# Kernel tuning notes

Measured on AMD Instinct MI355X. Metric: run time of the kernel, lower is better.

The kernel has to match this reference:

```python
import jax, jax.numpy as jnp
import numpy as np


def setup_inputs() -> dict:
    key = jax.random.key(0)
    ks = jax.random.split(key, 9)
    B, C, H, W = 4, 256, 64, 64
    Ci = C // 2
    s = 0.05  # keep activations numerically tame
    return {
        "x": jax.random.normal(ks[0], (B, C, H, W), jnp.float32),
        "w_g": jax.random.normal(ks[1], (Ci, C), jnp.float32) * s,
        "b_g": jax.random.normal(ks[2], (Ci,), jnp.float32) * s,
        "w_theta": jax.random.normal(ks[3], (Ci, C), jnp.float32) * s,
        "b_theta": jax.random.normal(ks[4], (Ci,), jnp.float32) * s,
        "w_phi": jax.random.normal(ks[5], (Ci, C), jnp.float32) * s,
        "b_phi": jax.random.normal(ks[6], (Ci,), jnp.float32) * s,
        "w_out": jax.random.normal(ks[7], (C, Ci), jnp.float32) * s,
        "b_out": jax.random.normal(ks[8], (C,), jnp.float32) * s,
    }


def reference(x, w_g, b_g, w_theta, b_theta, w_phi, b_phi, w_out, b_out):
    B, C, H, W = x.shape
    Ci = w_g.shape[0]
    N = H * W
    xr = x.reshape(B, C, N)  # flatten spatial dims

    def proj(w, b):  # 1x1 conv == per-pixel GEMM
        return jnp.einsum("oc,bcn->bon", w, xr) + b[None, :, None]

    g_x = proj(w_g, b_g)          # [B, Ci, N]
    theta_x = proj(w_theta, b_theta)
    phi_x = proj(w_phi, b_phi)

    scale = jnp.asarray(Ci, x.dtype) ** 0.5
    f = jnp.einsum("bci,bcj->bij", theta_x, phi_x) / scale  # [B, N, N]
    attn = jax.nn.softmax(f, axis=-1)

    # out[b,c,i] = sum_j g_x[b,c,j] * attn[b,i,j]
    out = jnp.einsum("bcj,bij->bci", g_x, attn)             # [B, Ci, N]
    y = jnp.einsum("oc,bcn->bon", w_out, out) + b_out[None, :, None]
    return y.reshape(B, C, H, W) + x
```

## Files before the change

### kernel.cpp

```cpp
#include <hip/hip_runtime.h>
#include <hip/hip_bf16.h>


typedef float f32x4 __attribute__((ext_vector_type(4)));
typedef short s16x8 __attribute__((ext_vector_type(8)));

#define B_  4
#define C_  256
#define CI_ 128
#define N_  4096

#define OFF_XT   0ull
#define OFF_Q    (8ull  << 20)
#define OFF_K    (12ull << 20)
#define OFF_G    (16ull << 20)
#define OFF_O    (20ull << 20)
#define OFF_WQK  (24ull << 20)
#define OFF_WG   (OFF_WQK + 131072)
#define OFF_WOUT (OFF_WG  + 65536)
#define OFF_BQK  (OFF_WOUT + 65536)
#define OFF_BG   (OFF_BQK + 1024)
#define OFF_BOUT (OFF_BG  + 512)
#define OFF_END  (OFF_BOUT + 1024)

__device__ inline f32x4 mfma16(s16x8 a, s16x8 b, f32x4 c) {
    return __builtin_amdgcn_mfma_f32_16x16x32_bf16(a, b, c, 0, 0, 0);
}
__device__ inline s16x8 ld8(const __hip_bfloat16* p) { return *(const s16x8*)p; }
__device__ inline float b2f(short u) {
    return __uint_as_float(((unsigned int)(unsigned short)u) << 16);
}
__device__ inline unsigned int pk2(float a, float b) {
    __hip_bfloat162 h;
    h.x = __float2bfloat16(a); h.y = __float2bfloat16(b);
    return *(unsigned int*)&h;
}
__device__ inline void gload_lds16(const void* g, void* l) {
    __builtin_amdgcn_global_load_lds(
        (const __attribute__((address_space(1))) unsigned int*)g,
        (__attribute__((address_space(3))) unsigned int*)l, 16, 0, 0);
}
__device__ inline float fexp2(float x) { return __builtin_amdgcn_exp2f(x); }

__global__ void prep_weights(const float* wg, const float* bg,
                             const float* wt, const float* bt,
                             const float* wp, const float* bp,
                             const float* wo, const float* bo, char* ws) {
    __hip_bfloat16* Wqk  = (__hip_bfloat16*)(ws + OFF_WQK);
    __hip_bfloat16* Wg   = (__hip_bfloat16*)(ws + OFF_WG);
    __hip_bfloat16* Wout = (__hip_bfloat16*)(ws + OFF_WOUT);
    float* Bqk  = (float*)(ws + OFF_BQK);
    float* Bg   = (float*)(ws + OFF_BG);
    float* Bout = (float*)(ws + OFF_BOUT);
    const float rs = 0.08838834764831845f * 1.4426950408889634f;
    int idx = blockIdx.x * 256 + threadIdx.x;
    if (idx < 65536) {
        int r = idx >> 8, c = idx & 255;
        float v = (r < 128) ? wt[r * 256 + c] * rs : wp[(r - 128) * 256 + c];
        Wqk[idx] = __float2bfloat16(v);
    }
    if (idx < 32768) {
        Wg[idx]   = __float2bfloat16(wg[idx]);
        Wout[idx] = __float2bfloat16(wo[idx]);
    }
    if (idx < 256) { Bqk[idx] = (idx < 128) ? bt[idx] * rs : bp[idx - 128]; Bout[idx] = bo[idx]; }
    if (idx < 128) Bg[idx] = bg[idx];
}

__global__ __launch_bounds__(256) void transpose_x(const float* x, char* ws) {
    __shared__ float tile[32][33];
    __hip_bfloat16* XT = (__hip_bfloat16*)(ws + OFF_XT);
    int b = blockIdx.z;
    int n0 = blockIdx.x * 32, c0 = blockIdx.y * 32;
    int tx = threadIdx.x & 31, ty = threadIdx.x >> 5;
#pragma unroll
    for (int r = 0; r < 4; r++)
        tile[ty + 8 * r][tx] = x[(size_t)(b * C_ + c0 + ty + 8 * r) * N_ + n0 + tx];
    __syncthreads();
#pragma unroll
    for (int r = 0; r < 4; r++)
        XT[(size_t)(b * N_ + n0 + ty + 8 * r) * C_ + c0 + tx] =
            __float2bfloat16(tile[tx][ty + 8 * r]);
}

__global__ __launch_bounds__(256) void proj(char* ws) {
    const __hip_bfloat16* XT  = (const __hip_bfloat16*)(ws + OFF_XT);
    const __hip_bfloat16* Wqk = (const __hip_bfloat16*)(ws + OFF_WQK);
    const __hip_bfloat16* Wg  = (const __hip_bfloat16*)(ws + OFF_WG);
    const float* Bqk = (const float*)(ws + OFF_BQK);
    const float* Bg  = (const float*)(ws + OFF_BG);
    __hip_bfloat16* Q  = (__hip_bfloat16*)(ws + OFF_Q);
    __hip_bfloat16* Kb = (__hip_bfloat16*)(ws + OFF_K);
    __hip_bfloat16* G  = (__hip_bfloat16*)(ws + OFF_G);

    __shared__ char at[32 * 512];

    int b = blockIdx.y, n0 = blockIdx.x * 32;
    int w = threadIdx.x >> 6, l = threadIdx.x & 63, lr = l & 15, lg = l >> 4;

    const char* xbase = (const char*)(XT + ((size_t)b * N_ + n0) * C_);
#pragma unroll
    for (int p = 0; p < 4; p++) {
        int row = p * 8 + w * 2 + (l >> 5);
        int slot = l & 31;
        const char* src = xbase + row * 512 + ((slot ^ (row & 7)) << 4);
        gload_lds16(src, &at[(p * 8 + w * 2) * 512]);
    }
    __syncthreads();

    f32x4 acc[4][2] = {};
    f32x4 accg[2][2] = {};
    int o0q = w * 64, o0g = w * 32;
#pragma unroll
    for (int kk = 0; kk < 8; kk++) {
        s16x8 a[2];
#pragma unroll
        for (int nf = 0; nf < 2; nf++) {
            int row = nf * 16 + lr;
            int s = (4 * kk + lg) ^ (row & 7);
            a[nf] = *(const s16x8*)(&at[row * 512 + s * 16]);
        }
#pragma unroll
        for (int of = 0; of < 4; of++) {
            s16x8 bb = ld8(Wqk + (size_t)(o0q + 16 * of + lr) * C_ + kk * 32 + lg * 8);
            acc[of][0] = mfma16(a[0], bb, acc[of][0]);
            acc[of][1] = mfma16(a[1], bb, acc[of][1]);
        }
#pragma unroll
        for (int og = 0; og < 2; og++) {
            s16x8 ag = ld8(Wg + (size_t)(o0g + 16 * og + lr) * C_ + kk * 32 + lg * 8);
            accg[og][0] = mfma16(ag, a[0], accg[og][0]);
            accg[og][1] = mfma16(ag, a[1], accg[og][1]);
        }
    }
#pragma unroll
    for (int of = 0; of < 4; of++) {
        int o = o0q + 16 * of + lr;
        float bias = Bqk[o];
#pragma unroll
        for (int nf = 0; nf < 2; nf++) {
#pragma unroll
            for (int i = 0; i < 4; i++) {
                int n = n0 + 16 * nf + lg * 4 + i;
                float v = acc[of][nf][i] + bias;
                if (o < 128) Q [(size_t)(b * N_ + n) * CI_ + o]         = __float2bfloat16(v);
                else         Kb[(size_t)(b * N_ + n) * CI_ + (o - 128)] = __float2bfloat16(v);
            }
        }
    }
#pragma unroll
    for (int og = 0; og < 2; og++) {
#pragma unroll
        for (int i = 0; i < 4; i++) {
            int o = o0g + 16 * og + lg * 4 + i;
            float bias = Bg[o];
#pragma unroll
            for (int nf = 0; nf < 2; nf++) {
                int n = n0 + 16 * nf + lr;
                G[(size_t)(b * CI_ + o) * N_ + n] = __float2bfloat16(accg[og][nf][i] + bias);
            }
        }
    }
}

__global__ __launch_bounds__(256, 3) void flash6(char* ws, int nchunk,
                                                 unsigned long long off_part,
                                                 unsigned long long off_ml) {
    const __hip_bfloat16* Q  = (const __hip_bfloat16*)(ws + OFF_Q);
    const __hip_bfloat16* Kb = (const __hip_bfloat16*)(ws + OFF_K);
    const __hip_bfloat16* G  = (const __hip_bfloat16*)(ws + OFF_G);
    __hip_bfloat16* OP = (__hip_bfloat16*)(ws + off_part);
    float* ML = (float*)(ws + off_ml);

    __shared__ char kbuf[2][32 * 256];
    __shared__ char vbuf[2][128 * 64];
    __shared__ char pbuf[4][2][2048];

    int L = blockIdx.x;
    int npairs = B_ * nchunk;
    int pair = L % npairs, qt = L / npairs;
    int b = pair / nchunk, cz = pair % nchunk;
    int per = 128 / nchunk, rem = 128 % nchunk;
    int jb_t = per * cz + (cz < rem ? cz : rem);
    int sz_t = per + (cz < rem ? 1 : 0);
    int jb = jb_t << 5, je = jb + (sz_t << 5);

    int w = threadIdx.x >> 6, l = threadIdx.x & 63, lr = l & 15, lg = l >> 4;
    int q0 = qt * 128 + w * 32;
    int swz = (lr & 7) << 4;
    char* pw = &pbuf[w][0][0];

    auto STAGE = [&](int pb_, int j0_) {
#pragma unroll
        for (int i = 0; i < 2; i++) {
            int row = w * 8 + i * 4 + (l >> 4);
            int bcol = ((l & 15) << 4) ^ ((row & 7) << 4);
            const char* src = (const char*)Kb + (((size_t)b * N_ + j0_ + row) << 8) + bcol;
            gload_lds16(src, &kbuf[pb_][(w * 8 + i * 4) * 256]);
        }
#pragma unroll
        for (int i = 0; i < 2; i++) {
            int c = w * 32 + i * 16 + (l >> 2);
            int joct = l & 3;
            const char* src = (const char*)G + ((((size_t)b * CI_ + c) * N_ + j0_) << 1)
                              + ((joct ^ (c & 3)) << 4);
            gload_lds16(src, &vbuf[pb_][(w * 32 + i * 16) * 64]);
        }
    };

    s16x8 qa[2][4];
#pragma unroll
    for (int qf = 0; qf < 2; qf++) {
        const __hip_bfloat16* qrow = Q + ((size_t)b * N_ + q0 + 16 * qf + lr) * CI_ + lg * 8;
#pragma unroll
        for (int kk = 0; kk < 4; kk++) qa[qf][kk] = ld8(qrow + kk * 32);
    }

    f32x4 oacc[2][8] = {};
    float m_i[2], lsum[2] = {0.f, 0.f};

    STAGE(0, jb);
    __syncthreads();
    int pb = 0;

    for (int j0 = jb; j0 < je; j0 += 32) {
        if (j0 + 32 < je) STAGE(pb ^ 1, j0 + 32);
        const char* kb = kbuf[pb];
        const char* vbb = vbuf[pb];
        f32x4 s[2][2] = {};
        __builtin_amdgcn_s_setprio(1);
#pragma unroll
        for (int kk = 0; kk < 4; kk++) {
            int bc = ((kk << 6) + (lg << 4)) ^ swz;
            s16x8 kf0 = *(const s16x8*)(kb + lr * 256 + bc);
            s16x8 kf1 = *(const s16x8*)(kb + (16 + lr) * 256 + bc);
            s[0][0] = mfma16(kf0, qa[0][kk], s[0][0]);
            s[1][0] = mfma16(kf0, qa[1][kk], s[1][0]);
            s[0][1] = mfma16(kf1, qa[0][kk], s[0][1]);
            s[1][1] = mfma16(kf1, qa[1][kk], s[1][1]);
        }
        __builtin_amdgcn_s_setprio(0);
        if (j0 == jb) {
#pragma unroll
            for (int qf = 0; qf < 2; qf++) {
                f32x4 m4;
                m4[0] = fmaxf(s[qf][0][0], s[qf][1][0]);
                m4[1] = fmaxf(s[qf][0][1], s[qf][1][1]);
                m4[2] = fmaxf(s[qf][0][2], s[qf][1][2]);
                m4[3] = fmaxf(s[qf][0][3], s[qf][1][3]);
                float tm = fmaxf(fmaxf(m4[0], m4[1]), fmaxf(m4[2], m4[3]));
                tm = fmaxf(tm, __shfl_xor(tm, 16));
                tm = fmaxf(tm, __shfl_xor(tm, 32));
                m_i[qf] = tm;
            }
        }
#pragma unroll
        for (int qf = 0; qf < 2; qf++) {
            float mref = m_i[qf];
            f32x4 sum4 = {};
#pragma unroll
            for (int t = 0; t < 2; t++) {
#pragma unroll
                for (int i = 0; i < 4; i++) s[qf][t][i] = fexp2(s[qf][t][i] - mref);
                sum4 += s[qf][t];
            }
            lsum[qf] += (sum4[0] + sum4[1]) + (sum4[2] + sum4[3]);
            char* base = pw + qf * 2048 + lr * 128;
#pragma unroll
            for (int t = 0; t < 2; t++) {
                unsigned int lo = pk2(s[qf][t][0], s[qf][t][1]);
                unsigned int hi = pk2(s[qf][t][2], s[qf][t][3]);
                int byte0 = ((t << 5) + (lg << 3)) ^ swz;
                *(unsigned int*)(base + byte0)     = lo;
                *(unsigned int*)(base + byte0 + 4) = hi;
            }
        }
        s16x8 pa0 = *(const s16x8*)(pw + lr * 128 + ((lg << 4) ^ swz));
        s16x8 pa1 = *(const s16x8*)(pw + 2048 + lr * 128 + ((lg << 4) ^ swz));
        __builtin_amdgcn_s_setprio(1);
#pragma unroll
        for (int cf = 0; cf < 8; cf++) {
            s16x8 vb = *(const s16x8*)(vbb + ((16 * cf + lr) << 6) +
                                       ((lg ^ (lr & 3)) << 4));
            oacc[0][cf] = mfma16(pa0, vb, oacc[0][cf]);
            oacc[1][cf] = mfma16(pa1, vb, oacc[1][cf]);
        }
        __builtin_amdgcn_s_setprio(0);
        __syncthreads();
        pb ^= 1;
    }
    float l_i[2];
#pragma unroll
    for (int qf = 0; qf < 2; qf++) {
        float rs = lsum[qf];
        rs += __shfl_xor(rs, 16);
        rs += __shfl_xor(rs, 32);
        l_i[qf] = rs;
    }
#pragma unroll
    for (int qf = 0; qf < 2; qf++) {
#pragma unroll
        for (int i = 0; i < 4; i++) {
            size_t row = ((size_t)(cz * B_ + b) * N_ + q0 + 16 * qf + lg * 4 + i) * CI_;
#pragma unroll
            for (int cf = 0; cf < 8; cf++)
                OP[row + 16 * cf + lr] = __float2bfloat16(oacc[qf][cf][i]);
        }
        if (lg == 0) {
            size_t mi = ((size_t)(cz * B_ + b) * N_ + q0 + 16 * qf + lr) * 2;
            ML[mi] = m_i[qf];
            ML[mi + 1] = l_i[qf];
        }
    }
}

template <int NC>
__global__ __launch_bounds__(256) void combine(char* ws,
                                               unsigned long long off_part,
                                               unsigned long long off_ml) {
    const __hip_bfloat16* OP = (const __hip_bfloat16*)(ws + off_part);
    const float* ML = (const float*)(ws + off_ml);
    __hip_bfloat16* O = (__hip_bfloat16*)(ws + OFF_O);
    int idx = blockIdx.x * 256 + threadIdx.x;
    int cg = idx & 15, n = (idx >> 4) & (N_ - 1), b = idx >> 16;
    float mz[NC], lz[NC], M = -1e30f;
#pragma unroll
    for (int z = 0; z < NC; z++) {
        size_t mi = ((size_t)(z * B_ + b) * N_ + n) * 2;
        mz[z] = ML[mi]; lz[z] = ML[mi + 1];
        M = fmaxf(M, mz[z]);
    }
    float Lsum = 0.f, wz[NC];
#pragma unroll
    for (int z = 0; z < NC; z++) { wz[z] = exp2f(mz[z] - M); Lsum += lz[z] * wz[z]; }
    float inv = 1.f / Lsum;
    float o[8] = {};
#pragma unroll
    for (int z = 0; z < NC; z++) {
        s16x8 v = ld8(OP + ((size_t)(z * B_ + b) * N_ + n) * CI_ + cg * 8);
#pragma unroll
        for (int i = 0; i < 8; i++) o[i] += wz[z] * b2f(v[i]);
    }
    s16x8 r;
#pragma unroll
    for (int i = 0; i < 8; i++) {
        __hip_bfloat16 h = __float2bfloat16(o[i] * inv);
        r[i] = *(short*)&h;
    }
    *(s16x8*)(O + ((size_t)b * N_ + n) * CI_ + cg * 8) = r;
}

__global__ __launch_bounds__(256) void gemm_out(const float* x, char* ws, float* y) {
    const __hip_bfloat16* Ob = (const __hip_bfloat16*)(ws + OFF_O);
    const __hip_bfloat16* Wo = (const __hip_bfloat16*)(ws + OFF_WOUT);
    const float* Bout = (const float*)(ws + OFF_BOUT);
    int b = blockIdx.y;
    int w = threadIdx.x >> 6, l = threadIdx.x & 63, lr = l & 15, lg = l >> 4;
    int n0 = blockIdx.x * 64;
    f32x4 acc[4][4] = {};
#pragma unroll
    for (int kk = 0; kk < 4; kk++) {
        s16x8 bb[4];
#pragma unroll
        for (int nf = 0; nf < 4; nf++)
            bb[nf] = ld8(Ob + (size_t)(b * N_ + n0 + 16 * nf + lr) * CI_ + kk * 32 + lg * 8);
#pragma unroll
        for (int f2 = 0; f2 < 4; f2++) {
            s16x8 a = ld8(Wo + (size_t)(w * 16 + f2 * 64 + lr) * CI_ + kk * 32 + lg * 8);
#pragma unroll
            for (int nf = 0; nf < 4; nf++)
                acc[f2][nf] = mfma16(a, bb[nf], acc[f2][nf]);
        }
    }
#pragma unroll
    for (int f2 = 0; f2 < 4; f2++) {
#pragma unroll
        for (int i = 0; i < 4; i++) {
            int o = w * 16 + f2 * 64 + lg * 4 + i;
            float bias = Bout[o];
#pragma unroll
            for (int nf = 0; nf < 4; nf++) {
                int n = n0 + 16 * nf + lr;
                size_t idx = (size_t)(b * C_ + o) * N_ + n;
                y[idx] = acc[f2][nf][i] + bias + x[idx];
            }
        }
    }
}

extern "C" void kernel_launch(void* const* d_in, const int* in_sizes, int n_in,
                              void* d_out, int out_size, void* d_ws, size_t ws_size,
                              hipStream_t stream) {
    const float* x  = (const float*)d_in[0];
    const float* wg = (const float*)d_in[1];
    const float* bg = (const float*)d_in[2];
    const float* wt = (const float*)d_in[3];
    const float* bt = (const float*)d_in[4];
    const float* wp = (const float*)d_in[5];
    const float* bp = (const float*)d_in[6];
    const float* wo = (const float*)d_in[7];
    const float* bo = (const float*)d_in[8];
    char* ws = (char*)d_ws;
    float* y = (float*)d_out;

    unsigned long long need6 = OFF_END + (24ull << 20) + (1ull << 20);
    unsigned long long need4 = OFF_END + (16ull << 20) + (1ull << 20);
    int nchunk;
    unsigned long long off_part, off_ml;
    if (ws_size >= need6) {
        nchunk = 6; off_part = OFF_END; off_ml = OFF_END + (24ull << 20);
    } else if (ws_size >= need4) {
        nchunk = 4; off_part = OFF_END; off_ml = OFF_END + (16ull << 20);
    } else {
        nchunk = 2; off_part = OFF_XT; off_ml = OFF_END;
    }

    prep_weights<<<256, 256, 0, stream>>>(wg, bg, wt, bt, wp, bp, wo, bo, ws);
    transpose_x<<<dim3(128, 8, 4), 256, 0, stream>>>(x, ws);
    proj<<<dim3(128, 4), 256, 0, stream>>>(ws);
    flash6<<<dim3(32 * B_ * nchunk), 256, 0, stream>>>(ws, nchunk, off_part, off_ml);
    if (nchunk == 6)      combine<6><<<1024, 256, 0, stream>>>(ws, off_part, off_ml);
    else if (nchunk == 4) combine<4><<<1024, 256, 0, stream>>>(ws, off_part, off_ml);
    else                  combine<2><<<1024, 256, 0, stream>>>(ws, off_part, off_ml);
    gemm_out<<<dim3(64, 4), 256, 0, stream>>>(x, ws, y);
}
```

Measured before the change: 101.7 us.

## Fuse split-KV combine into output GEMM and shrink P tile LDS swizzle

Removes the separate combine kernel by folding the split-chunk softmax rescaling and partial-output reduction into the output projection GEMM. The bf16 merged O tensor is no longer written and re-read, and one launch is dropped. Separately, the flash kernel's P staging buffer is halved, and a new swizzle is shared between the P tile and the V tile loads to cut LDS bank conflicts. In exchange, the fused GEMM does the per-pixel reduction redundantly across its 4 waves and has a larger prologue, which runs on only 256 blocks.

```diff
diff --git a/kernel.cpp b/kernel.cpp
--- a/kernel.cpp
+++ b/kernel.cpp
@@ -163,7 +163,7 @@
     }
 }
 
-__global__ __launch_bounds__(256, 3) void flash6(char* ws, int nchunk,
+__global__ __launch_bounds__(256, 3) void flash7(char* ws, int nchunk,
                                                  unsigned long long off_part,
                                                  unsigned long long off_ml) {
     const __hip_bfloat16* Q  = (const __hip_bfloat16*)(ws + OFF_Q);
@@ -174,7 +174,7 @@
 
     __shared__ char kbuf[2][32 * 256];
     __shared__ char vbuf[2][128 * 64];
-    __shared__ char pbuf[4][2][2048];
+    __shared__ char pbuf[4][2][1024];
 
     int L = blockIdx.x;
     int npairs = B_ * nchunk;
@@ -187,7 +187,8 @@
 
     int w = threadIdx.x >> 6, l = threadIdx.x & 63, lr = l & 15, lg = l >> 4;
     int q0 = qt * 128 + w * 32;
-    int swz = (lr & 7) << 4;
+    int swz  = (lr & 7) << 4;
+    int pswz = ((lr >> 1) & 3) << 4;
     char* pw = &pbuf[w][0][0];
 
     auto STAGE = [&](int pb_, int j0_) {
@@ -201,9 +202,9 @@
 #pragma unroll
         for (int i = 0; i < 2; i++) {
             int c = w * 32 + i * 16 + (l >> 2);
-            int joct = l & 3;
+            int srcslot = (l & 3) ^ ((l >> 3) & 3);
             const char* src = (const char*)G + ((((size_t)b * CI_ + c) * N_ + j0_) << 1)
-                              + ((joct ^ (c & 3)) << 4);
+                              + (srcslot << 4);
             gload_lds16(src, &vbuf[pb_][(w * 32 + i * 16) * 64]);
         }
     };
@@ -265,23 +266,24 @@
                 sum4 += s[qf][t];
             }
             lsum[qf] += (sum4[0] + sum4[1]) + (sum4[2] + sum4[3]);
-            char* base = pw + qf * 2048 + lr * 128;
+            char* base = pw + qf * 1024 + lr * 64;
 #pragma unroll
             for (int t = 0; t < 2; t++) {
                 unsigned int lo = pk2(s[qf][t][0], s[qf][t][1]);
                 unsigned int hi = pk2(s[qf][t][2], s[qf][t][3]);
-                int byte0 = ((t << 5) + (lg << 3)) ^ swz;
+                int slot = t * 2 + (lg >> 1);
+                int byte0 = ((slot << 4) ^ pswz) + ((lg & 1) << 3);
                 *(unsigned int*)(base + byte0)     = lo;
                 *(unsigned int*)(base + byte0 + 4) = hi;
             }
         }
-        s16x8 pa0 = *(const s16x8*)(pw + lr * 128 + ((lg << 4) ^ swz));
-        s16x8 pa1 = *(const s16x8*)(pw + 2048 + lr * 128 + ((lg << 4) ^ swz));
+        s16x8 pa0 = *(const s16x8*)(pw + lr * 64 + ((lg << 4) ^ pswz));
+        s16x8 pa1 = *(const s16x8*)(pw + 1024 + lr * 64 + ((lg << 4) ^ pswz));
         __builtin_amdgcn_s_setprio(1);
 #pragma unroll
         for (int cf = 0; cf < 8; cf++) {
             s16x8 vb = *(const s16x8*)(vbb + ((16 * cf + lr) << 6) +
-                                       ((lg ^ (lr & 3)) << 4));
+                                       ((lg << 4) ^ pswz));
             oacc[0][cf] = mfma16(pa0, vb, oacc[0][cf]);
             oacc[1][cf] = mfma16(pa1, vb, oacc[1][cf]);
         }
@@ -315,55 +317,61 @@
 }
 
 template <int NC>
-__global__ __launch_bounds__(256) void combine(char* ws,
-                                               unsigned long long off_part,
-                                               unsigned long long off_ml) {
+__global__ __launch_bounds__(256) void out_fused(const float* x, char* ws, float* y,
+                                                 unsigned long long off_part,
+                                                 unsigned long long off_ml) {
     const __hip_bfloat16* OP = (const __hip_bfloat16*)(ws + off_part);
     const float* ML = (const float*)(ws + off_ml);
-    __hip_bfloat16* O = (__hip_bfloat16*)(ws + OFF_O);
-    int idx = blockIdx.x * 256 + threadIdx.x;
-    int cg = idx & 15, n = (idx >> 4) & (N_ - 1), b = idx >> 16;
-    float mz[NC], lz[NC], M = -1e30f;
-#pragma unroll
-    for (int z = 0; z < NC; z++) {
-        size_t mi = ((size_t)(z * B_ + b) * N_ + n) * 2;
-        mz[z] = ML[mi]; lz[z] = ML[mi + 1];
-        M = fmaxf(M, mz[z]);
-    }
-    float Lsum = 0.f, wz[NC];
-#pragma unroll
-    for (int z = 0; z < NC; z++) { wz[z] = exp2f(mz[z] - M); Lsum += lz[z] * wz[z]; }
-    float inv = 1.f / Lsum;
-    float o[8] = {};
-#pragma unroll
-    for (int z = 0; z < NC; z++) {
-        s16x8 v = ld8(OP + ((size_t)(z * B_ + b) * N_ + n) * CI_ + cg * 8);
-#pragma unroll
-        for (int i = 0; i < 8; i++) o[i] += wz[z] * b2f(v[i]);
-    }
-    s16x8 r;
-#pragma unroll
-    for (int i = 0; i < 8; i++) {
-        __hip_bfloat16 h = __float2bfloat16(o[i] * inv);
-        r[i] = *(short*)&h;
-    }
-    *(s16x8*)(O + ((size_t)b * N_ + n) * CI_ + cg * 8) = r;
-}
-
-__global__ __launch_bounds__(256) void gemm_out(const float* x, char* ws, float* y) {
-    const __hip_bfloat16* Ob = (const __hip_bfloat16*)(ws + OFF_O);
     const __hip_bfloat16* Wo = (const __hip_bfloat16*)(ws + OFF_WOUT);
     const float* Bout = (const float*)(ws + OFF_BOUT);
     int b = blockIdx.y;
     int w = threadIdx.x >> 6, l = threadIdx.x & 63, lr = l & 15, lg = l >> 4;
     int n0 = blockIdx.x * 64;
+    float wz[4][NC];
+#pragma unroll
+    for (int nf = 0; nf < 4; nf++) {
+        int n = n0 + 16 * nf + lr;
+        float mz[NC], lz[NC], M = -1e30f;
+#pragma unroll
+        for (int z = 0; z < NC; z++) {
+            size_t mi = ((size_t)(z * B_ + b) * N_ + n) * 2;
+            mz[z] = ML[mi]; lz[z] = ML[mi + 1];
+            M = fmaxf(M, mz[z]);
+        }
+        float Ls = 0.f;
+#pragma unroll
+        for (int z = 0; z < NC; z++) {
+            float e = fexp2(mz[z] - M);
+            wz[nf][z] = e;
+            Ls += lz[z] * e;
+        }
+        float inv = 1.f / Ls;
+#pragma unroll
+        for (int z = 0; z < NC; z++) wz[nf][z] *= inv;
+    }
     f32x4 acc[4][4] = {};
 #pragma unroll
     for (int kk = 0; kk < 4; kk++) {
         s16x8 bb[4];
 #pragma unroll
-        for (int nf = 0; nf < 4; nf++)
-            bb[nf] = ld8(Ob + (size_t)(b * N_ + n0 + 16 * nf + lr) * CI_ + kk * 32 + lg * 8);
+        for (int nf = 0; nf < 4; nf++) {
+            int n = n0 + 16 * nf + lr;
+            float o8[8] = {};
+#pragma unroll
+            for (int z = 0; z < NC; z++) {
+                s16x8 v = ld8(OP + ((size_t)(z * B_ + b) * N_ + n) * CI_ + kk * 32 + lg * 8);
+                float wv = wz[nf][z];
+#pragma unroll
+                for (int e = 0; e < 8; e++) o8[e] += wv * b2f(v[e]);
+            }
+            s16x8 r;
+#pragma unroll
+            for (int e = 0; e < 8; e++) {
+                __hip_bfloat16 h = __float2bfloat16(o8[e]);
+                r[e] = *(short*)&h;
+            }
+            bb[nf] = r;
+        }
 #pragma unroll
         for (int f2 = 0; f2 < 4; f2++) {
             s16x8 a = ld8(Wo + (size_t)(w * 16 + f2 * 64 + lr) * CI_ + kk * 32 + lg * 8);
@@ -418,9 +426,11 @@
     prep_weights<<<256, 256, 0, stream>>>(wg, bg, wt, bt, wp, bp, wo, bo, ws);
     transpose_x<<<dim3(128, 8, 4), 256, 0, stream>>>(x, ws);
     proj<<<dim3(128, 4), 256, 0, stream>>>(ws);
-    flash6<<<dim3(32 * B_ * nchunk), 256, 0, stream>>>(ws, nchunk, off_part, off_ml);
-    if (nchunk == 6)      combine<6><<<1024, 256, 0, stream>>>(ws, off_part, off_ml);
-    else if (nchunk == 4) combine<4><<<1024, 256, 0, stream>>>(ws, off_part, off_ml);
-    else                  combine<2><<<1024, 256, 0, stream>>>(ws, off_part, off_ml);
-    gemm_out<<<dim3(64, 4), 256, 0, stream>>>(x, ws, y);
-}
+    flash7<<<dim3(32 * B_ * nchunk), 256, 0, stream>>>(ws, nchunk, off_part, off_ml);
+    if (nchunk == 6)
+        out_fused<6><<<dim3(64, 4), 256, 0, stream>>>(x, ws, y, off_part, off_ml);
+    else if (nchunk == 4)
+        out_fused<4><<<dim3(64, 4), 256, 0, stream>>>(x, ws, y, off_part, off_ml);
+    else
+        out_fused<2><<<dim3(64, 4), 256, 0, stream>>>(x, ws, y, off_part, off_ml);
+}
```

New measurement: 103.6 us. About the same (+1.9%).

## Switch flash attention to 32x32x16 MFMA and keep P in registers

Applied to the files above, without the earlier changes.

Rewrites the attention inner loop to use 32x32x16 bf16 MFMA tiles, so each wave computes its 32x32 score block with one accumulator. The S accumulator layout then matches the A-operand layout of the P·V MFMA, which removes the per-wave LDS round trip for P (the pbuf write, read and swizzle). The V staging swizzle and read pattern are changed to fit the new fragment shape. The combine kernel also folds the 1/L normalisation into the per-chunk weights and uses the hardware exp2. Risks are higher register pressure from the 16-wide accumulators under the 3-blocks-per-SM launch bound, and LDS bank conflicts from the new 8-byte V reads.

```diff
diff --git a/kernel.cpp b/kernel.cpp
--- a/kernel.cpp
+++ b/kernel.cpp
@@ -3,7 +3,9 @@
 
 
 typedef float f32x4 __attribute__((ext_vector_type(4)));
+typedef float f32x16 __attribute__((ext_vector_type(16)));
 typedef short s16x8 __attribute__((ext_vector_type(8)));
+typedef short s16x4 __attribute__((ext_vector_type(4)));
 
 #define B_  4
 #define C_  256
@@ -25,6 +27,9 @@
 
 __device__ inline f32x4 mfma16(s16x8 a, s16x8 b, f32x4 c) {
     return __builtin_amdgcn_mfma_f32_16x16x32_bf16(a, b, c, 0, 0, 0);
+}
+__device__ inline f32x16 mfma32(s16x8 a, s16x8 b, f32x16 c) {
+    return __builtin_amdgcn_mfma_f32_32x32x16_bf16(a, b, c, 0, 0, 0);
 }
 __device__ inline s16x8 ld8(const __hip_bfloat16* p) { return *(const s16x8*)p; }
 __device__ inline float b2f(short u) {
@@ -163,7 +168,7 @@
     }
 }
 
-__global__ __launch_bounds__(256, 3) void flash6(char* ws, int nchunk,
+__global__ __launch_bounds__(256, 3) void flash9(char* ws, int nchunk,
                                                  unsigned long long off_part,
                                                  unsigned long long off_ml) {
     const __hip_bfloat16* Q  = (const __hip_bfloat16*)(ws + OFF_Q);
@@ -174,7 +179,6 @@
 
     __shared__ char kbuf[2][32 * 256];
     __shared__ char vbuf[2][128 * 64];
-    __shared__ char pbuf[4][2][2048];
 
     int L = blockIdx.x;
     int npairs = B_ * nchunk;
@@ -185,10 +189,11 @@
     int sz_t = per + (cz < rem ? 1 : 0);
     int jb = jb_t << 5, je = jb + (sz_t << 5);
 
-    int w = threadIdx.x >> 6, l = threadIdx.x & 63, lr = l & 15, lg = l >> 4;
+    int w = threadIdx.x >> 6, l = threadIdx.x & 63;
+    int cl = l & 31, hi = l >> 5;
     int q0 = qt * 128 + w * 32;
-    int swz = (lr & 7) << 4;
-    char* pw = &pbuf[w][0][0];
+    int kkey = (l & 7) << 4;
+    int vkey = (l >> 1) & 3;
 
     auto STAGE = [&](int pb_, int j0_) {
 #pragma unroll
@@ -201,23 +206,22 @@
 #pragma unroll
         for (int i = 0; i < 2; i++) {
             int c = w * 32 + i * 16 + (l >> 2);
-            int joct = l & 3;
+            int srcslot = (l & 3) ^ ((l >> 3) & 3);
             const char* src = (const char*)G + ((((size_t)b * CI_ + c) * N_ + j0_) << 1)
-                              + ((joct ^ (c & 3)) << 4);
+                              + (srcslot << 4);
             gload_lds16(src, &vbuf[pb_][(w * 32 + i * 16) * 64]);
         }
     };
 
-    s16x8 qa[2][4];
-#pragma unroll
-    for (int qf = 0; qf < 2; qf++) {
-        const __hip_bfloat16* qrow = Q + ((size_t)b * N_ + q0 + 16 * qf + lr) * CI_ + lg * 8;
-#pragma unroll
-        for (int kk = 0; kk < 4; kk++) qa[qf][kk] = ld8(qrow + kk * 32);
-    }
-
-    f32x4 oacc[2][8] = {};
-    float m_i[2], lsum[2] = {0.f, 0.f};
+    s16x8 qb[8];
+    {
+        const __hip_bfloat16* qrow = Q + ((size_t)b * N_ + q0 + cl) * CI_ + hi * 8;
+#pragma unroll
+        for (int st = 0; st < 8; st++) qb[st] = ld8(qrow + st * 16);
+    }
+
+    f32x16 oacc[4] = {};
+    float m_i = 0.f, lsum = 0.f;
 
     STAGE(0, jb);
     __syncthreads();
@@ -227,90 +231,64 @@
         if (j0 + 32 < je) STAGE(pb ^ 1, j0 + 32);
         const char* kb = kbuf[pb];
         const char* vbb = vbuf[pb];
-        f32x4 s[2][2] = {};
+        f32x16 s = {};
         __builtin_amdgcn_s_setprio(1);
 #pragma unroll
-        for (int kk = 0; kk < 4; kk++) {
-            int bc = ((kk << 6) + (lg << 4)) ^ swz;
-            s16x8 kf0 = *(const s16x8*)(kb + lr * 256 + bc);
-            s16x8 kf1 = *(const s16x8*)(kb + (16 + lr) * 256 + bc);
-            s[0][0] = mfma16(kf0, qa[0][kk], s[0][0]);
-            s[1][0] = mfma16(kf0, qa[1][kk], s[1][0]);
-            s[0][1] = mfma16(kf1, qa[0][kk], s[0][1]);
-            s[1][1] = mfma16(kf1, qa[1][kk], s[1][1]);
+        for (int st = 0; st < 8; st++) {
+            s16x8 kf = *(const s16x8*)(kb + cl * 256 + ((((st << 1) + hi) << 4) ^ kkey));
+            s = mfma32(kf, qb[st], s);
         }
         __builtin_amdgcn_s_setprio(0);
         if (j0 == jb) {
-#pragma unroll
-            for (int qf = 0; qf < 2; qf++) {
-                f32x4 m4;
-                m4[0] = fmaxf(s[qf][0][0], s[qf][1][0]);
-                m4[1] = fmaxf(s[qf][0][1], s[qf][1][1]);
-                m4[2] = fmaxf(s[qf][0][2], s[qf][1][2]);
-                m4[3] = fmaxf(s[qf][0][3], s[qf][1][3]);
-                float tm = fmaxf(fmaxf(m4[0], m4[1]), fmaxf(m4[2], m4[3]));
-                tm = fmaxf(tm, __shfl_xor(tm, 16));
-                tm = fmaxf(tm, __shfl_xor(tm, 32));
-                m_i[qf] = tm;
+            float t0 = fmaxf(fmaxf(s[0], s[1]), fmaxf(s[2], s[3]));
+            float t1 = fmaxf(fmaxf(s[4], s[5]), fmaxf(s[6], s[7]));
+            float t2 = fmaxf(fmaxf(s[8], s[9]), fmaxf(s[10], s[11]));
+            float t3 = fmaxf(fmaxf(s[12], s[13]), fmaxf(s[14], s[15]));
+            float tm = fmaxf(fmaxf(t0, t1), fmaxf(t2, t3));
+            tm = fmaxf(tm, __shfl_xor(tm, 32));
+            m_i = tm;
+        }
+#pragma unroll
+        for (int r = 0; r < 16; r++) s[r] = fexp2(s[r] - m_i);
+        lsum += ((s[0] + s[1]) + (s[2] + s[3])) + ((s[4] + s[5]) + (s[6] + s[7]))
+              + ((s[8] + s[9]) + (s[10] + s[11])) + ((s[12] + s[13]) + (s[14] + s[15]));
+        union { unsigned int u[4]; s16x8 v; } pa0, pa1;
+#pragma unroll
+        for (int i = 0; i < 4; i++) {
+            pa0.u[i] = pk2(s[2 * i], s[2 * i + 1]);
+            pa1.u[i] = pk2(s[8 + 2 * i], s[9 + 2 * i]);
+        }
+        __builtin_amdgcn_s_setprio(1);
+#pragma unroll
+        for (int u = 0; u < 2; u++) {
+            s16x8 pa = u ? pa1.v : pa0.v;
+#pragma unroll
+            for (int cb = 0; cb < 4; cb++) {
+                const char* base = vbb + ((cb * 32 + cl) << 6) + hi * 8;
+                union { s16x4 h[2]; s16x8 v; } vf;
+                vf.h[0] = *(const s16x4*)(base + ((((u << 1))     ^ vkey) << 4));
+                vf.h[1] = *(const s16x4*)(base + ((((u << 1) | 1) ^ vkey) << 4));
+                oacc[cb] = mfma32(pa, vf.v, oacc[cb]);
             }
-        }
-#pragma unroll
-        for (int qf = 0; qf < 2; qf++) {
-            float mref = m_i[qf];
-            f32x4 sum4 = {};
-#pragma unroll
-            for (int t = 0; t < 2; t++) {
-#pragma unroll
-                for (int i = 0; i < 4; i++) s[qf][t][i] = fexp2(s[qf][t][i] - mref);
-                sum4 += s[qf][t];
-            }
-            lsum[qf] += (sum4[0] + sum4[1]) + (sum4[2] + sum4[3]);
-            char* base = pw + qf * 2048 + lr * 128;
-#pragma unroll
-            for (int t = 0; t < 2; t++) {
-                unsigned int lo = pk2(s[qf][t][0], s[qf][t][1]);
-                unsigned int hi = pk2(s[qf][t][2], s[qf][t][3]);
-                int byte0 = ((t << 5) + (lg << 3)) ^ swz;
-                *(unsigned int*)(base + byte0)     = lo;
-                *(unsigned int*)(base + byte0 + 4) = hi;
-            }
-        }
-        s16x8 pa0 = *(const s16x8*)(pw + lr * 128 + ((lg << 4) ^ swz));
-        s16x8 pa1 = *(const s16x8*)(pw + 2048 + lr * 128 + ((lg << 4) ^ swz));
-        __builtin_amdgcn_s_setprio(1);
-#pragma unroll
-        for (int cf = 0; cf < 8; cf++) {
-            s16x8 vb = *(const s16x8*)(vbb + ((16 * cf + lr) << 6) +
-                                       ((lg ^ (lr & 3)) << 4));
-            oacc[0][cf] = mfma16(pa0, vb, oacc[0][cf]);
-            oacc[1][cf] = mfma16(pa1, vb, oacc[1][cf]);
         }
         __builtin_amdgcn_s_setprio(0);
         __syncthreads();
         pb ^= 1;
     }
-    float l_i[2];
-#pragma unroll
-    for (int qf = 0; qf < 2; qf++) {
-        float rs = lsum[qf];
-        rs += __shfl_xor(rs, 16);
-        rs += __shfl_xor(rs, 32);
-        l_i[qf] = rs;
-    }
-#pragma unroll
-    for (int qf = 0; qf < 2; qf++) {
-#pragma unroll
-        for (int i = 0; i < 4; i++) {
-            size_t row = ((size_t)(cz * B_ + b) * N_ + q0 + 16 * qf + lg * 4 + i) * CI_;
-#pragma unroll
-            for (int cf = 0; cf < 8; cf++)
-                OP[row + 16 * cf + lr] = __float2bfloat16(oacc[qf][cf][i]);
-        }
-        if (lg == 0) {
-            size_t mi = ((size_t)(cz * B_ + b) * N_ + q0 + 16 * qf + lr) * 2;
-            ML[mi] = m_i[qf];
-            ML[mi + 1] = l_i[qf];
-        }
+    lsum += __shfl_xor(lsum, 32);
+#pragma unroll
+    for (int cb = 0; cb < 4; cb++) {
+#pragma unroll
+        for (int r = 0; r < 16; r++) {
+            int q = q0 + (r & 3) + 8 * (r >> 2) + 4 * hi;
+            OP[((size_t)(cz * B_ + b) * N_ + q) * CI_ + cb * 32 + cl] =
+                __float2bfloat16(oacc[cb][r]);
+        }
+    }
+    if (l < 32) {
+        size_t mi = ((size_t)(cz * B_ + b) * N_ + q0 + l) * 2;
+        ML[mi] = m_i;
+        ML[mi + 1] = lsum;
     }
 }
 
@@ -332,19 +310,20 @@
     }
     float Lsum = 0.f, wz[NC];
 #pragma unroll
-    for (int z = 0; z < NC; z++) { wz[z] = exp2f(mz[z] - M); Lsum += lz[z] * wz[z]; }
+    for (int z = 0; z < NC; z++) { wz[z] = fexp2(mz[z] - M); Lsum += lz[z] * wz[z]; }
     float inv = 1.f / Lsum;
     float o[8] = {};
 #pragma unroll
     for (int z = 0; z < NC; z++) {
         s16x8 v = ld8(OP + ((size_t)(z * B_ + b) * N_ + n) * CI_ + cg * 8);
-#pragma unroll
-        for (int i = 0; i < 8; i++) o[i] += wz[z] * b2f(v[i]);
+        float wv = wz[z] * inv;
+#pragma unroll
+        for (int i = 0; i < 8; i++) o[i] += wv * b2f(v[i]);
     }
     s16x8 r;
 #pragma unroll
     for (int i = 0; i < 8; i++) {
-        __hip_bfloat16 h = __float2bfloat16(o[i] * inv);
+        __hip_bfloat16 h = __float2bfloat16(o[i]);
         r[i] = *(short*)&h;
     }
     *(s16x8*)(O + ((size_t)b * N_ + n) * CI_ + cg * 8) = r;
@@ -418,7 +397,7 @@
     prep_weights<<<256, 256, 0, stream>>>(wg, bg, wt, bt, wp, bp, wo, bo, ws);
     transpose_x<<<dim3(128, 8, 4), 256, 0, stream>>>(x, ws);
     proj<<<dim3(128, 4), 256, 0, stream>>>(ws);
-    flash6<<<dim3(32 * B_ * nchunk), 256, 0, stream>>>(ws, nchunk, off_part, off_ml);
+    flash9<<<dim3(32 * B_ * nchunk), 256, 0, stream>>>(ws, nchunk, off_part, off_ml);
     if (nchunk == 6)      combine<6><<<1024, 256, 0, stream>>>(ws, off_part, off_ml);
     else if (nchunk == 4) combine<4><<<1024, 256, 0, stream>>>(ws, off_part, off_ml);
     else                  combine<2><<<1024, 256, 0, stream>>>(ws, off_part, off_ml);
```

Result: slower. 103.8 us (+2.0%).
